# Kernel tuning notes

Hardware: AMD Instinct MI355X
Metric: run time of the kernel (lower is better)

Reference implementation:

```python
import jax, jax.numpy as jnp
import numpy as np

B, S, D = 1, 1024, 64
_EPS = 1e-15
_BND = 1.0 - 1e-7  # artanh domain clamp (mirrors geoopt projection)


def _sq(x):
    return jnp.sum(x * x, axis=-1, keepdims=True)


def _nrm(x):
    return jnp.sqrt(_sq(x) + _EPS)


def _normalize(x, axis, eps):
    n = jnp.sqrt(jnp.sum(x * x, axis=axis, keepdims=True))
    return x / jnp.maximum(n, eps)


def _mobius_add(x, y):
    x2, y2 = _sq(x), _sq(y)
    xy = jnp.sum(x * y, axis=-1, keepdims=True)
    num = (1.0 + 2.0 * xy + y2) * x + (1.0 - x2) * y
    den = 1.0 + 2.0 * xy + x2 * y2
    return num / jnp.maximum(den, _EPS)


def _expmap0(u):
    n = _nrm(u)
    return jnp.tanh(n) * u / n


def _logmap0(y):
    n = _nrm(y)
    return jnp.arctanh(jnp.clip(n, 0.0, _BND)) * y / n


def _dist(x, y):
    n = _nrm(_mobius_add(-x, y))[..., 0]
    return 2.0 * jnp.arctanh(jnp.clip(n, 0.0, _BND))


def _logmap(x, y):
    d = _mobius_add(-x, y)
    n = _nrm(d)
    lam = 2.0 / jnp.maximum(1.0 - _sq(x), _EPS)
    return (2.0 / lam) * jnp.arctanh(jnp.clip(n, 0.0, _BND)) * d / n


def _transp0back(x, v):
    return v / jnp.maximum(1.0 - _sq(x), _EPS)


def _forward(q_in, k_in, v_in, Wq, bq, Wk, bk, Wv, bv, Wo, bo,
             tau, gamma, tangent_scale, gumbel_u, v_rand_init):
    q = q_in @ Wq.T + bq
    k = k_in @ Wk.T + bk
    v = v_in @ Wv.T + bv

    q_hyp = _expmap0(q)   # [B,S,D]
    k_hyp = _expmap0(k)

    # all-pairs geodesic distances [B,S,S]
    dist = _dist(q_hyp[:, :, None, :], k_hyp[:, None, :, :])
    min_d = jnp.min(dist, axis=-1, keepdims=True)
    w_un = jnp.exp(-(dist - min_d))                         # unnormalized weights
    w_sum = jnp.sum(w_un, axis=-1, keepdims=True) + 1e-8
    w_probs = w_un / w_sum
    h = jnp.einsum('bqk,bkd->bqd', w_probs, v)

    # Einstein midpoint: weighted Euclidean centroid of pre-map keys -> manifold
    centroid_euc = jnp.einsum('bqk,bkd->bqd', w_un / w_sum, k)
    centroid_hyp = _expmap0(centroid_euc)                   # [B,S,D]

    c2k = _dist(centroid_hyp[:, :, None, :], k_hyp[:, None, :, :])  # [B,S,S]
    wnv = w_un / w_sum
    entropy = -jnp.sum(wnv * jnp.log(wnv + 1e-8), axis=-1, keepdims=True)
    eff_mass = jnp.exp(entropy)
    variance = jnp.sum(wnv * c2k ** 2, axis=-1, keepdims=True)
    tension = variance - tau * eff_mass                     # [B,S,1]

    # matrix-free TPCA power iteration on weighted local tangents
    k_local = _logmap(centroid_hyp[:, :, None, :], k_hyp[:, None, :, :])  # [B,S,S,D]
    weighted_k = k_local * jnp.sqrt(w_un[..., None] + 1e-8)
    v_r = _normalize(v_rand_init, axis=2, eps=1e-12)        # [B,S,D,1]
    for _ in range(3):
        proj = jnp.einsum('bqkd,bqdo->bqko', weighted_k, v_r)
        v_r = jnp.einsum('bqkd,bqko->bqdo', weighted_k, proj)
        v_r = _normalize(v_r, axis=2, eps=1e-12)
    w_proj_local = v_r[..., 0]                              # [B,S,D]
    w_proj_global = _transp0back(centroid_hyp, w_proj_local)

    q_tan = _logmap0(q_hyp)
    c_tan = _logmap0(centroid_hyp)
    fallback = _normalize(q_tan - c_tan, axis=-1, eps=1e-8)
    w_proj = jnp.where(variance > 1e-5, w_proj_global, fallback)

    h_norm = _nrm(h)
    h_comp = jnp.arcsinh(h_norm) * (h / (h_norm + 1e-8))

    # Pitchfork bifurcation (c = 1)
    x = jnp.sum(h_comp * w_proj, axis=-1, keepdims=True)
    diss = (tension > 0).astype(h.dtype)
    h_mag = _nrm(h_comp)
    amplitude = h_mag * jnp.tanh(tension) * diss
    g = -jnp.log(-jnp.log(gumbel_u))                        # gumbel noise, logits = 0
    y_soft = jax.nn.softmax(g / 0.5, axis=-1)
    y_hard = jax.nn.one_hot(jnp.argmax(y_soft, axis=-1), 2, dtype=h.dtype)
    gp = y_soft + jax.lax.stop_gradient(y_hard - y_soft)    # straight-through
    eps_g = (gp[..., 0] - gp[..., 1])[..., None]            # gp @ [1,-1]
    x_star = eps_g * amplitude
    delta_c = jnp.tanh(x_star - x)
    h_prime = h_comp + delta_c * w_proj
    hp_norm = _nrm(h_prime) + 1e-8
    h_pb = h_prime * (jnp.tanh(hp_norm * tangent_scale) / hp_norm)
    h_prime_hyp = _expmap0(h_pb)

    h_out_bif = _logmap0(h_prime_hyp)
    gate = jax.nn.sigmoid(gamma)
    h_fused = (1.0 - gate) * h + gate * h_out_bif
    return h_fused @ Wo.T + bo


def setup_inputs() -> dict:
    key = jax.random.key(0)
    ks = jax.random.split(key, 10)
    std = 0.02
    return {
        'q_in': jax.random.normal(ks[0], (B, S, D), jnp.float32),
        'k_in': jax.random.normal(ks[1], (B, S, D), jnp.float32),
        'v_in': jax.random.normal(ks[2], (B, S, D), jnp.float32),
        'Wq': std * jax.random.normal(ks[3], (D, D), jnp.float32),
        'bq': jnp.zeros((D,), jnp.float32),
        'Wk': std * jax.random.normal(ks[4], (D, D), jnp.float32),
        'bk': jnp.zeros((D,), jnp.float32),
        'Wv': std * jax.random.normal(ks[5], (D, D), jnp.float32),
        'bv': jnp.zeros((D,), jnp.float32),
        'Wo': std * jax.random.normal(ks[6], (D, D), jnp.float32),
        'bo': jnp.zeros((D,), jnp.float32),
        'tau': jnp.float32(5.0),
        'gamma': jnp.float32(0.0),
        'tangent_scale': jnp.float32(0.1),
        'gumbel_u': jax.random.uniform(ks[7], (B, S, 2), jnp.float32, 1e-6, 1.0 - 1e-6),
        'v_rand_init': jax.random.normal(ks[8], (B, S, D, 1), jnp.float32),
    }


def reference(q_in, k_in, v_in, Wq, bq, Wk, bk, Wv, bv, Wo, bo,
              tau, gamma, tangent_scale, gumbel_u, v_rand_init):
    return _forward(q_in, k_in, v_in, Wq, bq, Wk, bk, Wv, bv, Wo, bo,
                    tau, gamma, tangent_scale, gumbel_u, v_rand_init)
```

## Files before the change

### kernel.cpp

```cpp
#include <hip/hip_runtime.h>
#include <math.h>

#define S 1024
#define D 64
#define BND 0.99999994f
#define FINF 3.4e38f
#define C4(v,c) ((&(v).x)[c])

__device__ __forceinline__ float waveSum(float v){
  #pragma unroll
  for(int o=32;o>0;o>>=1) v += __shfl_xor(v,o,64);
  return v;
}
__device__ __forceinline__ float4 mk4(const float* a){
  float4 r; r.x=a[0]; r.y=a[1]; r.z=a[2]; r.w=a[3]; return r;
}
__device__ __forceinline__ float4 blockSum512_v4(float4 v, float4* red4){
  #pragma unroll
  for(int o=32;o>0;o>>=1){
    v.x+=__shfl_xor(v.x,o,64); v.y+=__shfl_xor(v.y,o,64);
    v.z+=__shfl_xor(v.z,o,64); v.w+=__shfl_xor(v.w,o,64);
  }
  const int wid=threadIdx.x>>6;
  __syncthreads();
  if((threadIdx.x&63)==0) red4[wid]=v;
  __syncthreads();
  float4 s={0.f,0.f,0.f,0.f};
  #pragma unroll
  for(int k=0;k<8;k++){ float4 r=red4[k]; s.x+=r.x; s.y+=r.y; s.z+=r.z; s.w+=r.w; }
  return s;
}
__device__ __forceinline__ float4 blockMin512_v4(float4 v, float4* red4){
  #pragma unroll
  for(int o=32;o>0;o>>=1){
    v.x=fminf(v.x,__shfl_xor(v.x,o,64)); v.y=fminf(v.y,__shfl_xor(v.y,o,64));
    v.z=fminf(v.z,__shfl_xor(v.z,o,64)); v.w=fminf(v.w,__shfl_xor(v.w,o,64));
  }
  const int wid=threadIdx.x>>6;
  __syncthreads();
  if((threadIdx.x&63)==0) red4[wid]=v;
  __syncthreads();
  float4 s=red4[0];
  #pragma unroll
  for(int k=1;k<8;k++){ float4 r=red4[k]; s.x=fminf(s.x,r.x); s.y=fminf(s.y,r.y); s.z=fminf(s.z,r.z); s.w=fminf(s.w,r.w); }
  return s;
}

__global__ __launch_bounds__(64) void k_proj(
  const float* __restrict__ qin, const float* __restrict__ kin, const float* __restrict__ vin,
  const float* __restrict__ Wq, const float* __restrict__ bq,
  const float* __restrict__ Wk, const float* __restrict__ bk,
  const float* __restrict__ Wv, const float* __restrict__ bv,
  const float* __restrict__ vrand,
  float* __restrict__ q_hyp, float* __restrict__ k_hyp, float* __restrict__ kT,
  float* __restrict__ vproj, float* __restrict__ kproj,
  float* __restrict__ q2, float* __restrict__ k2, float* __restrict__ v_r)
{
  const int i = blockIdx.x, d = threadIdx.x;
  __shared__ __align__(16) float lq[D], lk[D], lv[D];
  lq[d]=qin[i*D+d]; lk[d]=kin[i*D+d]; lv[d]=vin[i*D+d];
  __syncthreads();
  float aq=bq[d], ak=bk[d], av=bv[d];
  const float4* wq4=(const float4*)(Wq + d*D);
  const float4* wk4=(const float4*)(Wk + d*D);
  const float4* wv4=(const float4*)(Wv + d*D);
  #pragma unroll
  for(int e=0;e<16;e++){
    float4 a=wq4[e], b=wk4[e], c=wv4[e];
    aq += lq[4*e]*a.x + lq[4*e+1]*a.y + lq[4*e+2]*a.z + lq[4*e+3]*a.w;
    ak += lk[4*e]*b.x + lk[4*e+1]*b.y + lk[4*e+2]*b.z + lk[4*e+3]*b.w;
    av += lv[4*e]*c.x + lv[4*e+1]*c.y + lv[4*e+2]*c.z + lv[4*e+3]*c.w;
  }
  float nq = sqrtf(waveSum(aq*aq)+1e-15f);
  float qh = tanhf(nq)*aq/nq;
  q_hyp[i*D+d]=qh;
  float q2v = waveSum(qh*qh);
  if(d==0) q2[i]=q2v;
  float nk = sqrtf(waveSum(ak*ak)+1e-15f);
  float kh = tanhf(nk)*ak/nk;
  k_hyp[i*D+d]=kh;
  kT[(size_t)d*S + i]=kh;
  float k2v = waveSum(kh*kh);
  if(d==0) k2[i]=k2v;
  vproj[i*D+d]=av;
  kproj[i*D+d]=ak;
  float vr = vrand[i*D+d];
  float nn = sqrtf(waveSum(vr*vr));
  v_r[i*D+d] = vr/fmaxf(nn,1e-12f);
}

__global__ __launch_bounds__(512,2) void k_fused(
  const float* __restrict__ q_hyp_g, const float* __restrict__ k_hyp,
  const float* __restrict__ kT,
  const float* __restrict__ q2a, const float* __restrict__ k2a,
  const float* __restrict__ vproj, const float* __restrict__ kproj,
  const float* __restrict__ v_r, const float* __restrict__ tau_p,
  const float* __restrict__ gu, const float* __restrict__ gamma_p,
  const float* __restrict__ ts_p, const float* __restrict__ Wo,
  const float* __restrict__ bo, float* __restrict__ out)
{
  const int i0=blockIdx.x*4, tid=threadIdx.x;
  __shared__ __align__(16) float qv[4][D];
  __shared__ __align__(16) float cv[4][D];
  __shared__ __align__(16) float vv[4][D];
  __shared__ __align__(16) float hl[4][D];
  __shared__ __align__(16) float fus[4][D];
  __shared__ __align__(16) float wl[4][S];
  __shared__ __align__(16) float aal[4][S];
  __shared__ __align__(16) float bbl[4][S];
  __shared__ __align__(16) float4 sA[2048];
  __shared__ __align__(16) float4 red4[8];
  __shared__ float scal[4][6];
  float* const pA=(float*)sA;

  if(tid<256){ qv[tid>>6][tid&63]=q_hyp_g[i0*D+tid]; vv[tid>>6][tid&63]=v_r[i0*D+tid]; }
  __syncthreads();

  const int jf=tid&255, dh=tid>>8;
  const int qq0=dh, qq1=dh+2;
  const int dq=tid&15, g=tid>>4;
  const float4* kT4=(const float4*)kT;
  const float tau=tau_p[0];

  {
    float4 p0={0,0,0,0},p1={0,0,0,0},p2={0,0,0,0},p3={0,0,0,0};
    #pragma unroll 8
    for(int dd=0; dd<32; ++dd){
      const int d=(dh<<5)+dd;
      const float4 y=kT4[d*256+jf];
      const float c0=qv[0][d], c1=qv[1][d], c2q=qv[2][d], c3=qv[3][d];
      p0.x+=c0*y.x; p0.y+=c0*y.y; p0.z+=c0*y.z; p0.w+=c0*y.w;
      p1.x+=c1*y.x; p1.y+=c1*y.y; p1.z+=c1*y.z; p1.w+=c1*y.w;
      p2.x+=c2q*y.x; p2.y+=c2q*y.y; p2.z+=c2q*y.z; p2.w+=c2q*y.w;
      p3.x+=c3*y.x; p3.y+=c3*y.y; p3.z+=c3*y.z; p3.w+=c3*y.w;
    }
    sA[(dh*4+0)*256+jf]=p0; sA[(dh*4+1)*256+jf]=p1;
    sA[(dh*4+2)*256+jf]=p2; sA[(dh*4+3)*256+jf]=p3;
  }
  __syncthreads();
  float4 inv4;
  {
    const float4 y2v=((const float4*)k2a)[jf];
    const float x2q[2]={q2a[i0+qq0], q2a[i0+qq1]};
    float dist[2][4];
    float4 mn4={FINF,FINF,FINF,FINF};
    #pragma unroll
    for(int it=0; it<2; ++it){
      const int qq = it? qq1:qq0;
      const float4 da=sA[(0*4+qq)*256+jf], db=sA[(1*4+qq)*256+jf];
      const float x2=x2q[it], B=1.f-x2;
      #pragma unroll
      for(int c=0;c<4;c++){
        const float y2=C4(y2v,c);
        const float dot=C4(da,c)+C4(db,c);
        const float A=1.f-2.f*dot+y2;
        const float den=fmaxf(1.f-2.f*dot+x2*y2,1e-15f);
        const float num2=fmaxf(A*A*x2 + B*B*y2 - 2.f*A*B*dot, 0.f);
        const float nn=sqrtf(num2/(den*den)+1e-15f);
        dist[it][c]=2.f*atanhf(fminf(nn,BND));
        C4(mn4,qq)=fminf(C4(mn4,qq),dist[it][c]);
      }
    }
    mn4=blockMin512_v4(mn4,red4);
    float w[2][4];
    float4 s4={0,0,0,0};
    #pragma unroll
    for(int it=0; it<2; ++it){
      const int qq = it? qq1:qq0;
      #pragma unroll
      for(int c=0;c<4;c++){ w[it][c]=expf(C4(mn4,qq)-dist[it][c]); C4(s4,qq)+=w[it][c]; }
      ((float4*)&wl[qq][0])[jf]=mk4(w[it]);
    }
    s4=blockSum512_v4(s4,red4);
    inv4.x=1.f/(s4.x+1e-8f); inv4.y=1.f/(s4.y+1e-8f);
    inv4.z=1.f/(s4.z+1e-8f); inv4.w=1.f/(s4.w+1e-8f);
    float4 e4={0,0,0,0};
    #pragma unroll
    for(int it=0; it<2; ++it){
      const int qq = it? qq1:qq0;
      #pragma unroll
      for(int c=0;c<4;c++){
        const float p=w[it][c]*C4(inv4,qq);
        C4(e4,qq) -= p*logf(p+1e-8f);
      }
    }
    e4=blockSum512_v4(e4,red4);
    if(tid<4) scal[tid][3]=expf(C4(e4,tid));
  }

  {
    float4 a0={0,0,0,0},a1={0,0,0,0},a2={0,0,0,0},a3={0,0,0,0};
    #pragma unroll 4
    for(int jj=0;jj<32;jj++){
      const int j=jj*32+g;
      const float4 y=((const float4*)(vproj + j*D))[dq];
      const float u0=wl[0][j],u1=wl[1][j],u2=wl[2][j],u3=wl[3][j];
      a0.x+=u0*y.x; a0.y+=u0*y.y; a0.z+=u0*y.z; a0.w+=u0*y.w;
      a1.x+=u1*y.x; a1.y+=u1*y.y; a1.z+=u1*y.z; a1.w+=u1*y.w;
      a2.x+=u2*y.x; a2.y+=u2*y.y; a2.z+=u2*y.z; a2.w+=u2*y.w;
      a3.x+=u3*y.x; a3.y+=u3*y.y; a3.z+=u3*y.z; a3.w+=u3*y.w;
    }
    __syncthreads();
    *(float4*)&pA[(g*4+0)*64+dq*4]=a0; *(float4*)&pA[(g*4+1)*64+dq*4]=a1;
    *(float4*)&pA[(g*4+2)*64+dq*4]=a2; *(float4*)&pA[(g*4+3)*64+dq*4]=a3;
    __syncthreads();
    if(tid<256){
      const int q=tid>>6, d=tid&63;
      float hs=0.f;
      #pragma unroll 8
      for(int gg=0;gg<32;gg++) hs+=pA[(gg*4+q)*64+d];
      hl[q][d]=hs*C4(inv4,q);
    }
    __syncthreads();
    float4 b0={0,0,0,0},b1={0,0,0,0},b2={0,0,0,0},b3={0,0,0,0};
    #pragma unroll 4
    for(int jj=0;jj<32;jj++){
      const int j=jj*32+g;
      const float4 y=((const float4*)(kproj + j*D))[dq];
      const float u0=wl[0][j],u1=wl[1][j],u2=wl[2][j],u3=wl[3][j];
      b0.x+=u0*y.x; b0.y+=u0*y.y; b0.z+=u0*y.z; b0.w+=u0*y.w;
      b1.x+=u1*y.x; b1.y+=u1*y.y; b1.z+=u1*y.z; b1.w+=u1*y.w;
      b2.x+=u2*y.x; b2.y+=u2*y.y; b2.z+=u2*y.z; b2.w+=u2*y.w;
      b3.x+=u3*y.x; b3.y+=u3*y.y; b3.z+=u3*y.z; b3.w+=u3*y.w;
    }
    *(float4*)&pA[(g*4+0)*64+dq*4]=b0; *(float4*)&pA[(g*4+1)*64+dq*4]=b1;
    *(float4*)&pA[(g*4+2)*64+dq*4]=b2; *(float4*)&pA[(g*4+3)*64+dq*4]=b3;
    __syncthreads();
    if(tid<256){
      const int q=tid>>6, d=tid&63;
      float cs=0.f;
      #pragma unroll 8
      for(int gg=0;gg<32;gg++) cs+=pA[(gg*4+q)*64+d];
      const float ca=cs*C4(inv4,q);
      const float n=sqrtf(waveSum(ca*ca)+1e-15f);
      const float ch=tanhf(n)*ca/n;
      cv[q][d]=ch;
      const float c2v=waveSum(ch*ch);
      if(d==0) scal[q][4]=c2v;
    }
  }
  __syncthreads();

  {
    float4 p0={0,0,0,0},p1={0,0,0,0},p2={0,0,0,0},p3={0,0,0,0};
    #pragma unroll 8
    for(int dd=0; dd<32; ++dd){
      const int d=(dh<<5)+dd;
      const float4 y=kT4[d*256+jf];
      const float c0=cv[0][d], c1=cv[1][d], c2q=cv[2][d], c3=cv[3][d];
      p0.x+=c0*y.x; p0.y+=c0*y.y; p0.z+=c0*y.z; p0.w+=c0*y.w;
      p1.x+=c1*y.x; p1.y+=c1*y.y; p1.z+=c1*y.z; p1.w+=c1*y.w;
      p2.x+=c2q*y.x; p2.y+=c2q*y.y; p2.z+=c2q*y.z; p2.w+=c2q*y.w;
      p3.x+=c3*y.x; p3.y+=c3*y.y; p3.z+=c3*y.z; p3.w+=c3*y.w;
    }
    sA[(dh*4+0)*256+jf]=p0; sA[(dh*4+1)*256+jf]=p1;
    sA[(dh*4+2)*256+jf]=p2; sA[(dh*4+3)*256+jf]=p3;
  }
  __syncthreads();
  {
    const float4 y2v=((const float4*)k2a)[jf];
    float4 var4={0,0,0,0};
    #pragma unroll
    for(int it=0; it<2; ++it){
      const int qq = it? qq1:qq0;
      const float4 da=sA[(0*4+qq)*256+jf], db=sA[(1*4+qq)*256+jf];
      const float4 wv=((float4*)&wl[qq][0])[jf];
      const float x2=scal[qq][4];
      const float Bc=1.f-x2, mB=fmaxf(Bc,1e-15f), inv=C4(inv4,qq);
      float ac[4], bc[4];
      #pragma unroll
      for(int c=0;c<4;c++){
        const float y2=C4(y2v,c);
        const float dot=C4(da,c)+C4(db,c);
        const float A=1.f-2.f*dot+y2;
        const float den=fmaxf(1.f-2.f*dot+x2*y2,1e-15f);
        const float num2=fmaxf(A*A*x2+Bc*Bc*y2-2.f*A*Bc*dot,0.f);
        const float nn=sqrtf(num2/(den*den)+1e-15f);
        const float art=atanhf(fminf(nn,BND));
        const float w=C4(wv,c);
        C4(var4,qq) += w*inv*4.f*art*art;
        const float coef=sqrtf(w+1e-8f)*mB*art/(nn*den);
        ac[c]=-coef*A; bc[c]=coef*Bc;
      }
      ((float4*)&aal[qq][0])[jf]=mk4(ac);
      ((float4*)&bbl[qq][0])[jf]=mk4(bc);
    }
    var4=blockSum512_v4(var4,red4);
    if(tid<4){ scal[tid][0]=C4(var4,tid); scal[tid][1]=C4(var4,tid) - tau*scal[tid][3]; }
  }
  float* const prow0=&wl[0][0];

  for(int it3=0; it3<3; ++it3){
    __syncthreads();
    if(tid<256){
      const int q=tid>>6, d=tid&63;
      const float cd=waveSum(cv[q][d]*vv[q][d]);
      if(d==0) scal[q][2]=cd;
    }
    __syncthreads();
    const float cd0=scal[0][2], cd1=scal[1][2], cd2=scal[2][2], cd3=scal[3][2];
    {
      float4 p0={0,0,0,0},p1={0,0,0,0},p2={0,0,0,0},p3={0,0,0,0};
      #pragma unroll 8
      for(int dd=0; dd<32; ++dd){
        const int d=(dh<<5)+dd;
        const float4 y=kT4[d*256+jf];
        const float c0=vv[0][d], c1=vv[1][d], c2q=vv[2][d], c3=vv[3][d];
        p0.x+=c0*y.x; p0.y+=c0*y.y; p0.z+=c0*y.z; p0.w+=c0*y.w;
        p1.x+=c1*y.x; p1.y+=c1*y.y; p1.z+=c1*y.z; p1.w+=c1*y.w;
        p2.x+=c2q*y.x; p2.y+=c2q*y.y; p2.z+=c2q*y.z; p2.w+=c2q*y.w;
        p3.x+=c3*y.x; p3.y+=c3*y.y; p3.z+=c3*y.z; p3.w+=c3*y.w;
      }
      sA[(dh*4+0)*256+jf]=p0; sA[(dh*4+1)*256+jf]=p1;
      sA[(dh*4+2)*256+jf]=p2; sA[(dh*4+3)*256+jf]=p3;
    }
    __syncthreads();
    float4 sal4={0,0,0,0};
    {
      const float cdq[2]={ dh? cd1:cd0, dh? cd3:cd2 };
      #pragma unroll
      for(int it=0; it<2; ++it){
        const int qq = it? qq1:qq0;
        const float4 da=sA[(0*4+qq)*256+jf], db=sA[(1*4+qq)*256+jf];
        const float4 av=((float4*)&aal[qq][0])[jf];
        const float4 bv=((float4*)&bbl[qq][0])[jf];
        float pr[4];
        #pragma unroll
        for(int c=0;c<4;c++){
          const float t=C4(da,c)+C4(db,c);
          const float p=C4(av,c)*cdq[it] + C4(bv,c)*t;
          pr[c]=p*C4(bv,c);
          C4(sal4,qq) += p*C4(av,c);
        }
        ((float4*)&prow0[qq*S])[jf]=mk4(pr);
      }
    }
    sal4=blockSum512_v4(sal4,red4);
    {
      float4 a0={0,0,0,0},a1={0,0,0,0},a2={0,0,0,0},a3={0,0,0,0};
      #pragma unroll 4
      for(int jj=0;jj<32;jj++){
        const int j=jj*32+g;
        const float4 y=((const float4*)(k_hyp + j*D))[dq];
        const float u0=prow0[0*S+j],u1=prow0[1*S+j],u2=prow0[2*S+j],u3=prow0[3*S+j];
        a0.x+=u0*y.x; a0.y+=u0*y.y; a0.z+=u0*y.z; a0.w+=u0*y.w;
        a1.x+=u1*y.x; a1.y+=u1*y.y; a1.z+=u1*y.z; a1.w+=u1*y.w;
        a2.x+=u2*y.x; a2.y+=u2*y.y; a2.z+=u2*y.z; a2.w+=u2*y.w;
        a3.x+=u3*y.x; a3.y+=u3*y.y; a3.z+=u3*y.z; a3.w+=u3*y.w;
      }
      *(float4*)&pA[(g*4+0)*64+dq*4]=a0; *(float4*)&pA[(g*4+1)*64+dq*4]=a1;
      *(float4*)&pA[(g*4+2)*64+dq*4]=a2; *(float4*)&pA[(g*4+3)*64+dq*4]=a3;
    }
    __syncthreads();
    if(tid<256){
      const int q=tid>>6, d=tid&63;
      float od=C4(sal4,q)*cv[q][d];
      #pragma unroll 8
      for(int gg=0;gg<32;gg++) od += pA[(gg*4+q)*64+d];
      const float nn=sqrtf(waveSum(od*od));
      vv[q][d]=od/fmaxf(nn,1e-12f);
    }
  }
  __syncthreads();

  if(tid<256){
    const int q=tid>>6, d=tid&63;
    const int i=i0+q;
    const float x2q_c=scal[q][4];
    const float vd=vv[q][d];
    const float vars=scal[q][0], tns=scal[q][1];
    const float hd=hl[q][d];
    const float qd=qv[q][d];
    const float q2=q2a[i];
    const float wpg=vd/fmaxf(1.f-x2q_c,1e-15f);
    const float nq=sqrtf(q2+1e-15f);
    const float qt=atanhf(fminf(nq,BND))*qd/nq;
    const float ncn=sqrtf(x2q_c+1e-15f);
    const float ct=atanhf(fminf(ncn,BND))*cv[q][d]/ncn;
    const float df=qt-ct;
    const float nd=sqrtf(waveSum(df*df));
    const float fb=df/fmaxf(nd,1e-8f);
    const float wp=(vars>1e-5f)?wpg:fb;
    const float hn=sqrtf(waveSum(hd*hd)+1e-15f);
    const float hc=asinhf(hn)*hd/(hn+1e-8f);
    const float x=waveSum(hc*wp);
    const float hmag=sqrtf(waveSum(hc*hc)+1e-15f);
    const float amp=(tns>0.f)? hmag*tanhf(tns) : 0.f;
    const float u0=gu[i*2], u1=gu[i*2+1];
    const float eg=(u0>=u1)?1.f:-1.f;
    const float dc=tanhf(eg*amp - x);
    const float hp=hc+dc*wp;
    const float hpn=sqrtf(waveSum(hp*hp)+1e-15f)+1e-8f;
    const float hpb=hp*(tanhf(hpn*ts_p[0])/hpn);
    const float n2=sqrtf(waveSum(hpb*hpb)+1e-15f);
    const float hyp=tanhf(n2)*hpb/n2;
    const float n3=sqrtf(waveSum(hyp*hyp)+1e-15f);
    const float bif=atanhf(fminf(n3,BND))*hyp/n3;
    const float gate=1.f/(1.f+expf(-gamma_p[0]));
    fus[q][d]=(1.f-gate)*hd + gate*bif;
  }
  __syncthreads();
  if(tid<256){
    const int q=tid>>6, d=tid&63;
    float acc=bo[d];
    const float4* wo4=(const float4*)(Wo + d*D);
    #pragma unroll
    for(int e=0;e<16;e++){
      float4 wv=wo4[e];
      acc += fus[q][4*e]*wv.x + fus[q][4*e+1]*wv.y + fus[q][4*e+2]*wv.z + fus[q][4*e+3]*wv.w;
    }
    out[(i0+q)*D+d]=acc;
  }
}

extern "C" void kernel_launch(void* const* d_in, const int* in_sizes, int n_in,
                              void* d_out, int out_size, void* d_ws, size_t ws_size,
                              hipStream_t stream)
{
  const float* qin=(const float*)d_in[0];
  const float* kin=(const float*)d_in[1];
  const float* vin=(const float*)d_in[2];
  const float* Wq=(const float*)d_in[3];
  const float* bq=(const float*)d_in[4];
  const float* Wk=(const float*)d_in[5];
  const float* bk=(const float*)d_in[6];
  const float* Wv=(const float*)d_in[7];
  const float* bv=(const float*)d_in[8];
  const float* Wo=(const float*)d_in[9];
  const float* bo=(const float*)d_in[10];
  const float* tau=(const float*)d_in[11];
  const float* gamma=(const float*)d_in[12];
  const float* tscale=(const float*)d_in[13];
  const float* gu=(const float*)d_in[14];
  const float* vrand=(const float*)d_in[15];
  float* out=(float*)d_out;

  float* p=(float*)d_ws;
  float* q_hyp=p; p+=S*D;
  float* k_hyp=p; p+=S*D;
  float* kT=p;    p+=S*D;
  float* vproj=p; p+=S*D;
  float* kproj=p; p+=S*D;
  float* v_r=p;   p+=S*D;
  float* q2=p;   p+=S;
  float* k2=p;   p+=S;

  k_proj<<<S,64,0,stream>>>(qin,kin,vin,Wq,bq,Wk,bk,Wv,bv,vrand,
                            q_hyp,k_hyp,kT,vproj,kproj,q2,k2,v_r);
  k_fused<<<S/4,512,0,stream>>>(q_hyp,k_hyp,kT,q2,k2,vproj,kproj,v_r,
                                tau,gu,gamma,tscale,Wo,bo,out);
}
```

Measured before the change: 89.96 us.

## Halve queries per block, interleave V/K projections, fuse reductions and syncs

The main kernel now handles 2 query rows per 512-thread block instead of 4, which doubles the grid to 512 blocks and raises the occupancy hint. The V and K projections are interleaved into one 128-wide buffer so a single weighted-sum pass produces both h and the centroid. Several block reductions are replaced with per-wave partials reduced later, which removes some barriers, and the projection kernel packs 4 rows per block. The cost is that the kT stream is re-read by twice as many blocks, and half the threads sit idle in the distance phases.

```diff
diff --git a/kernel.cpp b/kernel.cpp
--- a/kernel.cpp
+++ b/kernel.cpp
@@ -6,6 +6,7 @@
 #define BND 0.99999994f
 #define FINF 3.4e38f
 #define C4(v,c) ((&(v).x)[c])
+#define FMA4(acc,s,v) { (acc).x+=(s)*(v).x; (acc).y+=(s)*(v).y; (acc).z+=(s)*(v).z; (acc).w+=(s)*(v).w; }
 
 __device__ __forceinline__ float waveSum(float v){
   #pragma unroll
@@ -15,50 +16,45 @@
 __device__ __forceinline__ float4 mk4(const float* a){
   float4 r; r.x=a[0]; r.y=a[1]; r.z=a[2]; r.w=a[3]; return r;
 }
-__device__ __forceinline__ float4 blockSum512_v4(float4 v, float4* red4){
-  #pragma unroll
-  for(int o=32;o>0;o>>=1){
-    v.x+=__shfl_xor(v.x,o,64); v.y+=__shfl_xor(v.y,o,64);
-    v.z+=__shfl_xor(v.z,o,64); v.w+=__shfl_xor(v.w,o,64);
-  }
+__device__ __forceinline__ float2 blockSum512_v2(float2 v, float* red){
+  #pragma unroll
+  for(int o=32;o>0;o>>=1){ v.x+=__shfl_xor(v.x,o,64); v.y+=__shfl_xor(v.y,o,64); }
   const int wid=threadIdx.x>>6;
   __syncthreads();
-  if((threadIdx.x&63)==0) red4[wid]=v;
-  __syncthreads();
-  float4 s={0.f,0.f,0.f,0.f};
-  #pragma unroll
-  for(int k=0;k<8;k++){ float4 r=red4[k]; s.x+=r.x; s.y+=r.y; s.z+=r.z; s.w+=r.w; }
+  if((threadIdx.x&63)==0){ red[wid*2]=v.x; red[wid*2+1]=v.y; }
+  __syncthreads();
+  float2 s={0.f,0.f};
+  #pragma unroll
+  for(int k=0;k<8;k++){ s.x+=red[k*2]; s.y+=red[k*2+1]; }
   return s;
 }
-__device__ __forceinline__ float4 blockMin512_v4(float4 v, float4* red4){
-  #pragma unroll
-  for(int o=32;o>0;o>>=1){
-    v.x=fminf(v.x,__shfl_xor(v.x,o,64)); v.y=fminf(v.y,__shfl_xor(v.y,o,64));
-    v.z=fminf(v.z,__shfl_xor(v.z,o,64)); v.w=fminf(v.w,__shfl_xor(v.w,o,64));
-  }
+__device__ __forceinline__ float2 blockMin512_v2(float2 v, float* red){
+  #pragma unroll
+  for(int o=32;o>0;o>>=1){ v.x=fminf(v.x,__shfl_xor(v.x,o,64)); v.y=fminf(v.y,__shfl_xor(v.y,o,64)); }
   const int wid=threadIdx.x>>6;
   __syncthreads();
-  if((threadIdx.x&63)==0) red4[wid]=v;
-  __syncthreads();
-  float4 s=red4[0];
-  #pragma unroll
-  for(int k=1;k<8;k++){ float4 r=red4[k]; s.x=fminf(s.x,r.x); s.y=fminf(s.y,r.y); s.z=fminf(s.z,r.z); s.w=fminf(s.w,r.w); }
+  if((threadIdx.x&63)==0){ red[wid*2]=v.x; red[wid*2+1]=v.y; }
+  __syncthreads();
+  float2 s={red[0],red[1]};
+  #pragma unroll
+  for(int k=1;k<8;k++){ s.x=fminf(s.x,red[k*2]); s.y=fminf(s.y,red[k*2+1]); }
   return s;
 }
 
-__global__ __launch_bounds__(64) void k_proj(
+__global__ __launch_bounds__(256) void k_proj(
   const float* __restrict__ qin, const float* __restrict__ kin, const float* __restrict__ vin,
   const float* __restrict__ Wq, const float* __restrict__ bq,
   const float* __restrict__ Wk, const float* __restrict__ bk,
   const float* __restrict__ Wv, const float* __restrict__ bv,
   const float* __restrict__ vrand,
   float* __restrict__ q_hyp, float* __restrict__ k_hyp, float* __restrict__ kT,
-  float* __restrict__ vproj, float* __restrict__ kproj,
+  float* __restrict__ vk,
   float* __restrict__ q2, float* __restrict__ k2, float* __restrict__ v_r)
 {
-  const int i = blockIdx.x, d = threadIdx.x;
-  __shared__ __align__(16) float lq[D], lk[D], lv[D];
-  lq[d]=qin[i*D+d]; lk[d]=kin[i*D+d]; lv[d]=vin[i*D+d];
+  const int r=threadIdx.x>>6, d=threadIdx.x&63;
+  const int i = blockIdx.x*4+r;
+  __shared__ __align__(16) float lq[4][D], lk[4][D], lv[4][D];
+  lq[r][d]=qin[i*D+d]; lk[r][d]=kin[i*D+d]; lv[r][d]=vin[i*D+d];
   __syncthreads();
   float aq=bq[d], ak=bk[d], av=bv[d];
   const float4* wq4=(const float4*)(Wq + d*D);
@@ -67,9 +63,9 @@
   #pragma unroll
   for(int e=0;e<16;e++){
     float4 a=wq4[e], b=wk4[e], c=wv4[e];
-    aq += lq[4*e]*a.x + lq[4*e+1]*a.y + lq[4*e+2]*a.z + lq[4*e+3]*a.w;
-    ak += lk[4*e]*b.x + lk[4*e+1]*b.y + lk[4*e+2]*b.z + lk[4*e+3]*b.w;
-    av += lv[4*e]*c.x + lv[4*e+1]*c.y + lv[4*e+2]*c.z + lv[4*e+3]*c.w;
+    aq += lq[r][4*e]*a.x + lq[r][4*e+1]*a.y + lq[r][4*e+2]*a.z + lq[r][4*e+3]*a.w;
+    ak += lk[r][4*e]*b.x + lk[r][4*e+1]*b.y + lk[r][4*e+2]*b.z + lk[r][4*e+3]*b.w;
+    av += lv[r][4*e]*c.x + lv[r][4*e+1]*c.y + lv[r][4*e+2]*c.z + lv[r][4*e+3]*c.w;
   }
   float nq = sqrtf(waveSum(aq*aq)+1e-15f);
   float qh = tanhf(nq)*aq/nq;
@@ -82,293 +78,275 @@
   kT[(size_t)d*S + i]=kh;
   float k2v = waveSum(kh*kh);
   if(d==0) k2[i]=k2v;
-  vproj[i*D+d]=av;
-  kproj[i*D+d]=ak;
+  vk[(size_t)i*128 + d]      = av;
+  vk[(size_t)i*128 + 64 + d] = ak;
   float vr = vrand[i*D+d];
   float nn = sqrtf(waveSum(vr*vr));
   v_r[i*D+d] = vr/fmaxf(nn,1e-12f);
 }
 
-__global__ __launch_bounds__(512,2) void k_fused(
+__global__ __launch_bounds__(512,4) void k_main(
   const float* __restrict__ q_hyp_g, const float* __restrict__ k_hyp,
   const float* __restrict__ kT,
   const float* __restrict__ q2a, const float* __restrict__ k2a,
-  const float* __restrict__ vproj, const float* __restrict__ kproj,
-  const float* __restrict__ v_r, const float* __restrict__ tau_p,
+  const float* __restrict__ vk, const float* __restrict__ v_r,
+  const float* __restrict__ tau_p,
   const float* __restrict__ gu, const float* __restrict__ gamma_p,
   const float* __restrict__ ts_p, const float* __restrict__ Wo,
   const float* __restrict__ bo, float* __restrict__ out)
 {
-  const int i0=blockIdx.x*4, tid=threadIdx.x;
-  __shared__ __align__(16) float qv[4][D];
-  __shared__ __align__(16) float cv[4][D];
-  __shared__ __align__(16) float vv[4][D];
-  __shared__ __align__(16) float hl[4][D];
-  __shared__ __align__(16) float fus[4][D];
-  __shared__ __align__(16) float wl[4][S];
-  __shared__ __align__(16) float aal[4][S];
-  __shared__ __align__(16) float bbl[4][S];
-  __shared__ __align__(16) float4 sA[2048];
-  __shared__ __align__(16) float4 red4[8];
-  __shared__ float scal[4][6];
+  const int i0=blockIdx.x*2, tid=threadIdx.x;
+  __shared__ __align__(16) float qv[2][D];
+  __shared__ __align__(16) float cv[2][D];
+  __shared__ __align__(16) float vv[2][D];
+  __shared__ __align__(16) float hl[2][D];
+  __shared__ __align__(16) float fus[2][D];
+  __shared__ __align__(16) float wl[2][S];
+  __shared__ __align__(16) float aal[2][S];
+  __shared__ __align__(16) float bbl[2][S];
+  __shared__ __align__(16) float4 sA[1024];
+  __shared__ float red[16];
+  __shared__ float varred[16];
+  __shared__ float salred[16];
+  __shared__ float scal[2][4];
   float* const pA=(float*)sA;
 
-  if(tid<256){ qv[tid>>6][tid&63]=q_hyp_g[i0*D+tid]; vv[tid>>6][tid&63]=v_r[i0*D+tid]; }
-  __syncthreads();
-
   const int jf=tid&255, dh=tid>>8;
-  const int qq0=dh, qq1=dh+2;
   const int dq=tid&15, g=tid>>4;
+  const int dq5=tid&31, g16=tid>>5;
+  const float tau=tau_p[0];
   const float4* kT4=(const float4*)kT;
-  const float tau=tau_p[0];
+
+  if(tid<128){
+    const int q=tid>>6, d=tid&63;
+    qv[q][d]=q_hyp_g[i0*D+tid];
+    vv[q][d]=v_r[i0*D+tid];
+  }
+  __syncthreads();
 
   {
-    float4 p0={0,0,0,0},p1={0,0,0,0},p2={0,0,0,0},p3={0,0,0,0};
+    float4 p0={0,0,0,0}, p1={0,0,0,0};
     #pragma unroll 8
     for(int dd=0; dd<32; ++dd){
       const int d=(dh<<5)+dd;
       const float4 y=kT4[d*256+jf];
-      const float c0=qv[0][d], c1=qv[1][d], c2q=qv[2][d], c3=qv[3][d];
-      p0.x+=c0*y.x; p0.y+=c0*y.y; p0.z+=c0*y.z; p0.w+=c0*y.w;
-      p1.x+=c1*y.x; p1.y+=c1*y.y; p1.z+=c1*y.z; p1.w+=c1*y.w;
-      p2.x+=c2q*y.x; p2.y+=c2q*y.y; p2.z+=c2q*y.z; p2.w+=c2q*y.w;
-      p3.x+=c3*y.x; p3.y+=c3*y.y; p3.z+=c3*y.z; p3.w+=c3*y.w;
-    }
-    sA[(dh*4+0)*256+jf]=p0; sA[(dh*4+1)*256+jf]=p1;
-    sA[(dh*4+2)*256+jf]=p2; sA[(dh*4+3)*256+jf]=p3;
-  }
-  __syncthreads();
-  float4 inv4;
+      const float c0=qv[0][d], c1=qv[1][d];
+      FMA4(p0,c0,y); FMA4(p1,c1,y);
+    }
+    sA[(dh*2+0)*256+jf]=p0;
+    sA[(dh*2+1)*256+jf]=p1;
+  }
+  __syncthreads();
+  float2 sinv;
+  float2 effm2;
   {
-    const float4 y2v=((const float4*)k2a)[jf];
-    const float x2q[2]={q2a[i0+qq0], q2a[i0+qq1]};
     float dist[2][4];
-    float4 mn4={FINF,FINF,FINF,FINF};
-    #pragma unroll
-    for(int it=0; it<2; ++it){
-      const int qq = it? qq1:qq0;
-      const float4 da=sA[(0*4+qq)*256+jf], db=sA[(1*4+qq)*256+jf];
-      const float x2=x2q[it], B=1.f-x2;
+    float2 mn2={FINF,FINF};
+    if(tid<256){
+      const float4 y2v=((const float4*)k2a)[jf];
       #pragma unroll
-      for(int c=0;c<4;c++){
-        const float y2=C4(y2v,c);
-        const float dot=C4(da,c)+C4(db,c);
-        const float A=1.f-2.f*dot+y2;
-        const float den=fmaxf(1.f-2.f*dot+x2*y2,1e-15f);
-        const float num2=fmaxf(A*A*x2 + B*B*y2 - 2.f*A*B*dot, 0.f);
-        const float nn=sqrtf(num2/(den*den)+1e-15f);
-        dist[it][c]=2.f*atanhf(fminf(nn,BND));
-        C4(mn4,qq)=fminf(C4(mn4,qq),dist[it][c]);
-      }
-    }
-    mn4=blockMin512_v4(mn4,red4);
+      for(int q=0;q<2;q++){
+        const float x2=q2a[i0+q], B=1.f-x2;
+        const float4 da=sA[q*256+jf], db=sA[(2+q)*256+jf];
+        #pragma unroll
+        for(int c=0;c<4;c++){
+          const float y2=C4(y2v,c);
+          const float dot=C4(da,c)+C4(db,c);
+          const float A=1.f-2.f*dot+y2;
+          const float den=fmaxf(1.f-2.f*dot+x2*y2,1e-15f);
+          const float num2=fmaxf(A*A*x2 + B*B*y2 - 2.f*A*B*dot, 0.f);
+          const float nn=sqrtf(num2/(den*den)+1e-15f);
+          dist[q][c]=2.f*atanhf(fminf(nn,BND));
+          C4(mn2,q)=fminf(C4(mn2,q),dist[q][c]);
+        }
+      }
+    }
+    mn2=blockMin512_v2(mn2,red);
     float w[2][4];
-    float4 s4={0,0,0,0};
-    #pragma unroll
-    for(int it=0; it<2; ++it){
-      const int qq = it? qq1:qq0;
+    float2 s2={0.f,0.f};
+    if(tid<256){
       #pragma unroll
-      for(int c=0;c<4;c++){ w[it][c]=expf(C4(mn4,qq)-dist[it][c]); C4(s4,qq)+=w[it][c]; }
-      ((float4*)&wl[qq][0])[jf]=mk4(w[it]);
-    }
-    s4=blockSum512_v4(s4,red4);
-    inv4.x=1.f/(s4.x+1e-8f); inv4.y=1.f/(s4.y+1e-8f);
-    inv4.z=1.f/(s4.z+1e-8f); inv4.w=1.f/(s4.w+1e-8f);
-    float4 e4={0,0,0,0};
-    #pragma unroll
-    for(int it=0; it<2; ++it){
-      const int qq = it? qq1:qq0;
+      for(int q=0;q<2;q++){
+        #pragma unroll
+        for(int c=0;c<4;c++){ w[q][c]=expf(C4(mn2,q)-dist[q][c]); C4(s2,q)+=w[q][c]; }
+        ((float4*)&wl[q][0])[jf]=mk4(w[q]);
+      }
+    }
+    s2=blockSum512_v2(s2,red);
+    sinv.x=1.f/(s2.x+1e-8f); sinv.y=1.f/(s2.y+1e-8f);
+    float2 e2={0.f,0.f};
+    if(tid<256){
       #pragma unroll
-      for(int c=0;c<4;c++){
-        const float p=w[it][c]*C4(inv4,qq);
-        C4(e4,qq) -= p*logf(p+1e-8f);
-      }
-    }
-    e4=blockSum512_v4(e4,red4);
-    if(tid<4) scal[tid][3]=expf(C4(e4,tid));
+      for(int q=0;q<2;q++){
+        #pragma unroll
+        for(int c=0;c<4;c++){
+          const float p=w[q][c]*C4(sinv,q);
+          C4(e2,q) -= p*logf(p+1e-8f);
+        }
+      }
+    }
+    e2=blockSum512_v2(e2,red);
+    effm2.x=expf(e2.x); effm2.y=expf(e2.y);
   }
 
   {
-    float4 a0={0,0,0,0},a1={0,0,0,0},a2={0,0,0,0},a3={0,0,0,0};
+    float4 a0={0,0,0,0}, a1={0,0,0,0};
     #pragma unroll 4
-    for(int jj=0;jj<32;jj++){
-      const int j=jj*32+g;
-      const float4 y=((const float4*)(vproj + j*D))[dq];
-      const float u0=wl[0][j],u1=wl[1][j],u2=wl[2][j],u3=wl[3][j];
-      a0.x+=u0*y.x; a0.y+=u0*y.y; a0.z+=u0*y.z; a0.w+=u0*y.w;
-      a1.x+=u1*y.x; a1.y+=u1*y.y; a1.z+=u1*y.z; a1.w+=u1*y.w;
-      a2.x+=u2*y.x; a2.y+=u2*y.y; a2.z+=u2*y.z; a2.w+=u2*y.w;
-      a3.x+=u3*y.x; a3.y+=u3*y.y; a3.z+=u3*y.z; a3.w+=u3*y.w;
-    }
-    __syncthreads();
-    *(float4*)&pA[(g*4+0)*64+dq*4]=a0; *(float4*)&pA[(g*4+1)*64+dq*4]=a1;
-    *(float4*)&pA[(g*4+2)*64+dq*4]=a2; *(float4*)&pA[(g*4+3)*64+dq*4]=a3;
-    __syncthreads();
-    if(tid<256){
-      const int q=tid>>6, d=tid&63;
-      float hs=0.f;
-      #pragma unroll 8
-      for(int gg=0;gg<32;gg++) hs+=pA[(gg*4+q)*64+d];
-      hl[q][d]=hs*C4(inv4,q);
-    }
-    __syncthreads();
-    float4 b0={0,0,0,0},b1={0,0,0,0},b2={0,0,0,0},b3={0,0,0,0};
-    #pragma unroll 4
-    for(int jj=0;jj<32;jj++){
-      const int j=jj*32+g;
-      const float4 y=((const float4*)(kproj + j*D))[dq];
-      const float u0=wl[0][j],u1=wl[1][j],u2=wl[2][j],u3=wl[3][j];
-      b0.x+=u0*y.x; b0.y+=u0*y.y; b0.z+=u0*y.z; b0.w+=u0*y.w;
-      b1.x+=u1*y.x; b1.y+=u1*y.y; b1.z+=u1*y.z; b1.w+=u1*y.w;
-      b2.x+=u2*y.x; b2.y+=u2*y.y; b2.z+=u2*y.z; b2.w+=u2*y.w;
-      b3.x+=u3*y.x; b3.y+=u3*y.y; b3.z+=u3*y.z; b3.w+=u3*y.w;
-    }
-    *(float4*)&pA[(g*4+0)*64+dq*4]=b0; *(float4*)&pA[(g*4+1)*64+dq*4]=b1;
-    *(float4*)&pA[(g*4+2)*64+dq*4]=b2; *(float4*)&pA[(g*4+3)*64+dq*4]=b3;
-    __syncthreads();
-    if(tid<256){
-      const int q=tid>>6, d=tid&63;
-      float cs=0.f;
-      #pragma unroll 8
-      for(int gg=0;gg<32;gg++) cs+=pA[(gg*4+q)*64+d];
-      const float ca=cs*C4(inv4,q);
-      const float n=sqrtf(waveSum(ca*ca)+1e-15f);
-      const float ch=tanhf(n)*ca/n;
+    for(int jj=0;jj<64;jj++){
+      const int j=jj*16+g16;
+      const float4 y=((const float4*)(vk + (size_t)j*128))[dq5];
+      const float u0=wl[0][j], u1=wl[1][j];
+      FMA4(a0,u0,y); FMA4(a1,u1,y);
+    }
+    *(float4*)&pA[(g16*2+0)*128 + dq5*4]=a0;
+    *(float4*)&pA[(g16*2+1)*128 + dq5*4]=a1;
+  }
+  __syncthreads();
+  if(tid<256){
+    const int q=tid>>7, dd=tid&127;
+    float s=0.f;
+    #pragma unroll 8
+    for(int gg=0;gg<16;gg++) s+=pA[(gg*2+q)*128+dd];
+    s *= C4(sinv,q);
+    if(dd<64){
+      hl[q][dd]=s;
+    }else{
+      const int d=dd-64;
+      const float n=sqrtf(waveSum(s*s)+1e-15f);
+      const float ch=tanhf(n)*s/n;
       cv[q][d]=ch;
       const float c2v=waveSum(ch*ch);
-      if(d==0) scal[q][4]=c2v;
+      const float cd=waveSum(ch*vv[q][d]);
+      if(d==0){ scal[q][0]=c2v; scal[q][2]=cd; }
     }
   }
   __syncthreads();
 
   {
-    float4 p0={0,0,0,0},p1={0,0,0,0},p2={0,0,0,0},p3={0,0,0,0};
+    float4 p0={0,0,0,0}, p1={0,0,0,0};
     #pragma unroll 8
     for(int dd=0; dd<32; ++dd){
       const int d=(dh<<5)+dd;
       const float4 y=kT4[d*256+jf];
-      const float c0=cv[0][d], c1=cv[1][d], c2q=cv[2][d], c3=cv[3][d];
-      p0.x+=c0*y.x; p0.y+=c0*y.y; p0.z+=c0*y.z; p0.w+=c0*y.w;
-      p1.x+=c1*y.x; p1.y+=c1*y.y; p1.z+=c1*y.z; p1.w+=c1*y.w;
-      p2.x+=c2q*y.x; p2.y+=c2q*y.y; p2.z+=c2q*y.z; p2.w+=c2q*y.w;
-      p3.x+=c3*y.x; p3.y+=c3*y.y; p3.z+=c3*y.z; p3.w+=c3*y.w;
-    }
-    sA[(dh*4+0)*256+jf]=p0; sA[(dh*4+1)*256+jf]=p1;
-    sA[(dh*4+2)*256+jf]=p2; sA[(dh*4+3)*256+jf]=p3;
+      const float c0=cv[0][d], c1=cv[1][d];
+      FMA4(p0,c0,y); FMA4(p1,c1,y);
+    }
+    sA[(dh*2+0)*256+jf]=p0;
+    sA[(dh*2+1)*256+jf]=p1;
   }
   __syncthreads();
   {
-    const float4 y2v=((const float4*)k2a)[jf];
-    float4 var4={0,0,0,0};
-    #pragma unroll
-    for(int it=0; it<2; ++it){
-      const int qq = it? qq1:qq0;
-      const float4 da=sA[(0*4+qq)*256+jf], db=sA[(1*4+qq)*256+jf];
-      const float4 wv=((float4*)&wl[qq][0])[jf];
-      const float x2=scal[qq][4];
-      const float Bc=1.f-x2, mB=fmaxf(Bc,1e-15f), inv=C4(inv4,qq);
-      float ac[4], bc[4];
+    float var[2]={0.f,0.f};
+    if(tid<256){
+      const float4 y2v=((const float4*)k2a)[jf];
       #pragma unroll
-      for(int c=0;c<4;c++){
-        const float y2=C4(y2v,c);
-        const float dot=C4(da,c)+C4(db,c);
-        const float A=1.f-2.f*dot+y2;
-        const float den=fmaxf(1.f-2.f*dot+x2*y2,1e-15f);
-        const float num2=fmaxf(A*A*x2+Bc*Bc*y2-2.f*A*Bc*dot,0.f);
-        const float nn=sqrtf(num2/(den*den)+1e-15f);
-        const float art=atanhf(fminf(nn,BND));
-        const float w=C4(wv,c);
-        C4(var4,qq) += w*inv*4.f*art*art;
-        const float coef=sqrtf(w+1e-8f)*mB*art/(nn*den);
-        ac[c]=-coef*A; bc[c]=coef*Bc;
-      }
-      ((float4*)&aal[qq][0])[jf]=mk4(ac);
-      ((float4*)&bbl[qq][0])[jf]=mk4(bc);
-    }
-    var4=blockSum512_v4(var4,red4);
-    if(tid<4){ scal[tid][0]=C4(var4,tid); scal[tid][1]=C4(var4,tid) - tau*scal[tid][3]; }
-  }
+      for(int q=0;q<2;q++){
+        const float x2=scal[q][0];
+        const float Bc=1.f-x2, mB=fmaxf(Bc,1e-15f), inv=C4(sinv,q);
+        const float4 da=sA[q*256+jf], db=sA[(2+q)*256+jf];
+        const float4 wv=((float4*)&wl[q][0])[jf];
+        float ac[4], bc[4];
+        #pragma unroll
+        for(int c=0;c<4;c++){
+          const float y2=C4(y2v,c);
+          const float dot=C4(da,c)+C4(db,c);
+          const float A=1.f-2.f*dot+y2;
+          const float den=fmaxf(1.f-2.f*dot+x2*y2,1e-15f);
+          const float num2=fmaxf(A*A*x2+Bc*Bc*y2-2.f*A*Bc*dot,0.f);
+          const float nn=sqrtf(num2/(den*den)+1e-15f);
+          const float art=atanhf(fminf(nn,BND));
+          const float w=C4(wv,c);
+          var[q] += w*inv*4.f*art*art;
+          const float coef=sqrtf(w+1e-8f)*mB*art/(nn*den);
+          ac[c]=-coef*A; bc[c]=coef*Bc;
+        }
+        ((float4*)&aal[q][0])[jf]=mk4(ac);
+        ((float4*)&bbl[q][0])[jf]=mk4(bc);
+      }
+    }
+    const float v0=waveSum(var[0]), v1=waveSum(var[1]);
+    if((tid&63)==0){ varred[(tid>>6)*2]=v0; varred[(tid>>6)*2+1]=v1; }
+  }
+  __syncthreads();
   float* const prow0=&wl[0][0];
 
   for(int it3=0; it3<3; ++it3){
-    __syncthreads();
-    if(tid<256){
-      const int q=tid>>6, d=tid&63;
-      const float cd=waveSum(cv[q][d]*vv[q][d]);
-      if(d==0) scal[q][2]=cd;
-    }
-    __syncthreads();
-    const float cd0=scal[0][2], cd1=scal[1][2], cd2=scal[2][2], cd3=scal[3][2];
     {
-      float4 p0={0,0,0,0},p1={0,0,0,0},p2={0,0,0,0},p3={0,0,0,0};
+      float4 p0={0,0,0,0}, p1={0,0,0,0};
       #pragma unroll 8
       for(int dd=0; dd<32; ++dd){
         const int d=(dh<<5)+dd;
         const float4 y=kT4[d*256+jf];
-        const float c0=vv[0][d], c1=vv[1][d], c2q=vv[2][d], c3=vv[3][d];
-        p0.x+=c0*y.x; p0.y+=c0*y.y; p0.z+=c0*y.z; p0.w+=c0*y.w;
-        p1.x+=c1*y.x; p1.y+=c1*y.y; p1.z+=c1*y.z; p1.w+=c1*y.w;
-        p2.x+=c2q*y.x; p2.y+=c2q*y.y; p2.z+=c2q*y.z; p2.w+=c2q*y.w;
-        p3.x+=c3*y.x; p3.y+=c3*y.y; p3.z+=c3*y.z; p3.w+=c3*y.w;
-      }
-      sA[(dh*4+0)*256+jf]=p0; sA[(dh*4+1)*256+jf]=p1;
-      sA[(dh*4+2)*256+jf]=p2; sA[(dh*4+3)*256+jf]=p3;
+        const float c0=vv[0][d], c1=vv[1][d];
+        FMA4(p0,c0,y); FMA4(p1,c1,y);
+      }
+      sA[(dh*2+0)*256+jf]=p0;
+      sA[(dh*2+1)*256+jf]=p1;
     }
     __syncthreads();
-    float4 sal4={0,0,0,0};
     {
-      const float cdq[2]={ dh? cd1:cd0, dh? cd3:cd2 };
-      #pragma unroll
-      for(int it=0; it<2; ++it){
-        const int qq = it? qq1:qq0;
-        const float4 da=sA[(0*4+qq)*256+jf], db=sA[(1*4+qq)*256+jf];
-        const float4 av=((float4*)&aal[qq][0])[jf];
-        const float4 bv=((float4*)&bbl[qq][0])[jf];
-        float pr[4];
+      float sal[2]={0.f,0.f};
+      if(tid<256){
+        const float cdq[2]={scal[0][2], scal[1][2]};
         #pragma unroll
-        for(int c=0;c<4;c++){
-          const float t=C4(da,c)+C4(db,c);
-          const float p=C4(av,c)*cdq[it] + C4(bv,c)*t;
-          pr[c]=p*C4(bv,c);
-          C4(sal4,qq) += p*C4(av,c);
+        for(int q=0;q<2;q++){
+          const float4 da=sA[q*256+jf], db=sA[(2+q)*256+jf];
+          const float4 av=((float4*)&aal[q][0])[jf];
+          const float4 bv=((float4*)&bbl[q][0])[jf];
+          float pr[4];
+          #pragma unroll
+          for(int c=0;c<4;c++){
+            const float t=C4(da,c)+C4(db,c);
+            const float p=C4(av,c)*cdq[q] + C4(bv,c)*t;
+            pr[c]=p*C4(bv,c);
+            sal[q] += p*C4(av,c);
+          }
+          ((float4*)&prow0[q*S])[jf]=mk4(pr);
         }
-        ((float4*)&prow0[qq*S])[jf]=mk4(pr);
-      }
-    }
-    sal4=blockSum512_v4(sal4,red4);
+      }
+      const float s0=waveSum(sal[0]), s1=waveSum(sal[1]);
+      if((tid&63)==0){ salred[(tid>>6)*2]=s0; salred[(tid>>6)*2+1]=s1; }
+    }
+    __syncthreads();
     {
-      float4 a0={0,0,0,0},a1={0,0,0,0},a2={0,0,0,0},a3={0,0,0,0};
+      float4 a0={0,0,0,0}, a1={0,0,0,0};
       #pragma unroll 4
       for(int jj=0;jj<32;jj++){
         const int j=jj*32+g;
         const float4 y=((const float4*)(k_hyp + j*D))[dq];
-        const float u0=prow0[0*S+j],u1=prow0[1*S+j],u2=prow0[2*S+j],u3=prow0[3*S+j];
-        a0.x+=u0*y.x; a0.y+=u0*y.y; a0.z+=u0*y.z; a0.w+=u0*y.w;
-        a1.x+=u1*y.x; a1.y+=u1*y.y; a1.z+=u1*y.z; a1.w+=u1*y.w;
-        a2.x+=u2*y.x; a2.y+=u2*y.y; a2.z+=u2*y.z; a2.w+=u2*y.w;
-        a3.x+=u3*y.x; a3.y+=u3*y.y; a3.z+=u3*y.z; a3.w+=u3*y.w;
-      }
-      *(float4*)&pA[(g*4+0)*64+dq*4]=a0; *(float4*)&pA[(g*4+1)*64+dq*4]=a1;
-      *(float4*)&pA[(g*4+2)*64+dq*4]=a2; *(float4*)&pA[(g*4+3)*64+dq*4]=a3;
+        const float u0=prow0[0*S+j], u1=prow0[1*S+j];
+        FMA4(a0,u0,y); FMA4(a1,u1,y);
+      }
+      *(float4*)&pA[(g*2+0)*64+dq*4]=a0;
+      *(float4*)&pA[(g*2+1)*64+dq*4]=a1;
     }
     __syncthreads();
-    if(tid<256){
+    if(tid<128){
       const int q=tid>>6, d=tid&63;
-      float od=C4(sal4,q)*cv[q][d];
+      float salt=0.f;
+      #pragma unroll
+      for(int k=0;k<8;k++) salt+=salred[k*2+q];
+      float od=salt*cv[q][d];
       #pragma unroll 8
-      for(int gg=0;gg<32;gg++) od += pA[(gg*4+q)*64+d];
+      for(int gg=0;gg<32;gg++) od += pA[(gg*2+q)*64+d];
       const float nn=sqrtf(waveSum(od*od));
-      vv[q][d]=od/fmaxf(nn,1e-12f);
-    }
-  }
-  __syncthreads();
-
-  if(tid<256){
+      const float vn=od/fmaxf(nn,1e-12f);
+      vv[q][d]=vn;
+      const float cd=waveSum(cv[q][d]*vn);
+      if(d==0) scal[q][2]=cd;
+    }
+    __syncthreads();
+  }
+
+  if(tid<128){
     const int q=tid>>6, d=tid&63;
     const int i=i0+q;
-    const float x2q_c=scal[q][4];
+    float vart=0.f;
+    #pragma unroll
+    for(int k=0;k<8;k++) vart+=varred[k*2+q];
+    const float tns=vart - tau*C4(effm2,q);
+    const float x2q_c=scal[q][0];
     const float vd=vv[q][d];
-    const float vars=scal[q][0], tns=scal[q][1];
     const float hd=hl[q][d];
     const float qd=qv[q][d];
     const float q2=q2a[i];
@@ -380,7 +358,7 @@
     const float df=qt-ct;
     const float nd=sqrtf(waveSum(df*df));
     const float fb=df/fmaxf(nd,1e-8f);
-    const float wp=(vars>1e-5f)?wpg:fb;
+    const float wp=(vart>1e-5f)?wpg:fb;
     const float hn=sqrtf(waveSum(hd*hd)+1e-15f);
     const float hc=asinhf(hn)*hd/(hn+1e-8f);
     const float x=waveSum(hc*wp);
@@ -400,7 +378,7 @@
     fus[q][d]=(1.f-gate)*hd + gate*bif;
   }
   __syncthreads();
-  if(tid<256){
+  if(tid<128){
     const int q=tid>>6, d=tid&63;
     float acc=bo[d];
     const float4* wo4=(const float4*)(Wo + d*D);
@@ -439,14 +417,13 @@
   float* q_hyp=p; p+=S*D;
   float* k_hyp=p; p+=S*D;
   float* kT=p;    p+=S*D;
-  float* vproj=p; p+=S*D;
-  float* kproj=p; p+=S*D;
+  float* vk=p;    p+=(size_t)S*128;
   float* v_r=p;   p+=S*D;
   float* q2=p;   p+=S;
   float* k2=p;   p+=S;
 
-  k_proj<<<S,64,0,stream>>>(qin,kin,vin,Wq,bq,Wk,bk,Wv,bv,vrand,
-                            q_hyp,k_hyp,kT,vproj,kproj,q2,k2,v_r);
-  k_fused<<<S/4,512,0,stream>>>(q_hyp,k_hyp,kT,q2,k2,vproj,kproj,v_r,
-                                tau,gu,gamma,tscale,Wo,bo,out);
-}
+  k_proj<<<S/4,256,0,stream>>>(qin,kin,vin,Wq,bq,Wk,bk,Wv,bv,vrand,
+                               q_hyp,k_hyp,kT,vk,q2,k2,v_r);
+  k_main<<<S/2,512,0,stream>>>(q_hyp,k_hyp,kT,q2,k2,vk,v_r,
+                               tau,gu,gamma,tscale,Wo,bo,out);
+}
```

Result: slower. 95.17 us (+5.8%).
